# Kernel optimization log

Measured on AMD Instinct MI355X. Metric: run time of the kernel, lower is better.

## Reference

```python
import jax, jax.numpy as jnp
import numpy as np

N, F_IN, HID, NCLS, E = 50000, 128, 256, 40, 600000
BN_EPS = 1e-5


def setup_inputs() -> dict:
    key = jax.random.key(0)
    ks = jax.random.split(key, 12)
    x = jax.random.normal(ks[0], (N, F_IN), dtype=jnp.float32)
    edge_index = jax.random.randint(ks[1], (2, E), 0, N, dtype=jnp.int64)
    # BatchNorm0 (over input features) running stats + affine params
    bn0_gamma = jnp.ones((F_IN,), jnp.float32)
    bn0_beta = jnp.zeros((F_IN,), jnp.float32)
    bn0_mean = jax.random.normal(ks[2], (F_IN,), jnp.float32) * 0.1
    bn0_var = jax.random.uniform(ks[3], (F_IN,), jnp.float32, 0.5, 1.5)
    # GINConv1 linear: F_IN -> HID
    W1 = jax.random.normal(ks[4], (F_IN, HID), jnp.float32) / np.sqrt(F_IN)
    b1 = jnp.zeros((HID,), jnp.float32)
    # BatchNorm1 (over hidden)
    bn1_gamma = jnp.ones((HID,), jnp.float32)
    bn1_beta = jnp.zeros((HID,), jnp.float32)
    bn1_mean = jax.random.normal(ks[5], (HID,), jnp.float32) * 0.1
    bn1_var = jax.random.uniform(ks[6], (HID,), jnp.float32, 0.5, 1.5)
    # GINConv2 linear: HID -> NCLS
    W2 = jax.random.normal(ks[7], (HID, NCLS), jnp.float32) / np.sqrt(HID)
    b2 = jnp.zeros((NCLS,), jnp.float32)
    return {
        "x": x, "edge_index": edge_index,
        "bn0_gamma": bn0_gamma, "bn0_beta": bn0_beta,
        "bn0_mean": bn0_mean, "bn0_var": bn0_var,
        "W1": W1, "b1": b1,
        "bn1_gamma": bn1_gamma, "bn1_beta": bn1_beta,
        "bn1_mean": bn1_mean, "bn1_var": bn1_var,
        "W2": W2, "b2": b2,
    }


def _bn_eval(h, gamma, beta, mean, var):
    return (h - mean) * (gamma / jnp.sqrt(var + BN_EPS)) + beta


def _gin_agg(h, src, dst, n):
    # sum_{j in N(i)} h_j  (scatter-add over edges), plus self term (eps=0)
    return h + jax.ops.segment_sum(h[src], dst, num_segments=n)


def reference(x, edge_index, bn0_gamma, bn0_beta, bn0_mean, bn0_var,
              W1, b1, bn1_gamma, bn1_beta, bn1_mean, bn1_var, W2, b2):
    # Eval mode: dropout / dropout_edge are identity; BN uses running stats.
    src, dst = edge_index[0], edge_index[1]
    n = x.shape[0]
    h = _bn_eval(x, bn0_gamma, bn0_beta, bn0_mean, bn0_var)
    h = _gin_agg(h, src, dst, n) @ W1 + b1          # GINConv1
    h = _bn_eval(h, bn1_gamma, bn1_beta, bn1_mean, bn1_var)
    h = jax.nn.relu(h)
    out = _gin_agg(h, src, dst, n) @ W2 + b2        # GINConv2 -> logits [N, NCLS]
    return out
```

## Files before the change

### kernel.cpp

```cpp
#include <hip/hip_runtime.h>

#define NN 50000
#define FIN 128
#define HID 256
#define NCLS 40
#define NE 600000
#define BN_EPS 1e-5f
#define MAXDEG 64

typedef _Float16 half4_t __attribute__((ext_vector_type(4)));
typedef _Float16 half8_t __attribute__((ext_vector_type(8)));
typedef float float4_t __attribute__((ext_vector_type(4)));


#define OFF_DEG    1600000
#define OFF_GH     1650000
#define OFF_XH     3200000
#define OFF_W1T    6450000
#define OFF_W2T    6466384
#define OFF_P      6472528
#define OFF_Q      6472784
#define OFF_S0V    6473040
#define OFF_S1V    6473168
#define OFF_T0V    6473424

__global__ void scales_k(const float* __restrict__ bn0_g, const float* __restrict__ bn0_b,
                         const float* __restrict__ bn0_m, const float* __restrict__ bn0_v,
                         const float* __restrict__ b1,
                         const float* __restrict__ bn1_g, const float* __restrict__ bn1_b,
                         const float* __restrict__ bn1_m, const float* __restrict__ bn1_v,
                         float* __restrict__ s0v, float* __restrict__ s1v,
                         float* __restrict__ t0v, float* __restrict__ p, float* __restrict__ q) {
    int t = threadIdx.x;
    if (t < FIN) {
        float s = bn0_g[t] * rsqrtf(bn0_v[t] + BN_EPS);
        s0v[t] = s;
        t0v[t] = bn0_b[t] - bn0_m[t] * s;
    }
    float sc = bn1_g[t] * rsqrtf(bn1_v[t] + BN_EPS);
    s1v[t] = sc;
    p[t] = 0.f;
    q[t] = (b1[t] - bn1_m[t]) * sc + bn1_b[t];
}

__global__ void transpose_k(const float* __restrict__ W1, const float* __restrict__ W2,
                            const float* __restrict__ s0v, const float* __restrict__ s1v,
                            const float* __restrict__ t0v,
                            _Float16* __restrict__ W1T, _Float16* __restrict__ W2T,
                            float* __restrict__ p, int* __restrict__ deg) {
    int t = threadIdx.x;
    int b = blockIdx.x;
    if (b >= 9) {
        int i = (b - 9) * 256 + t;
        if (i < NN) deg[i] = 0;
        return;
    }
    if (b < 8) {
        __shared__ _Float16 T[64][65];
        int k0 = (b >> 2) * 64;
        int c0 = (b & 3) * 64;
        int cc = t & 63;
        float psum = 0.f;
        #pragma unroll
        for (int i = 0; i < 16; ++i) {
            int idx = i * 256 + t;
            int kk = idx >> 6;
            float w = W1[(size_t)(k0 + kk) * HID + c0 + cc];
            psum += t0v[k0 + kk] * w;
            T[cc][kk] = (_Float16)(w * s0v[k0 + kk] * s1v[c0 + cc]);
        }
        atomicAdd(&p[c0 + cc], psum * s1v[c0 + cc]);
        __syncthreads();
        #pragma unroll
        for (int i = 0; i < 16; ++i) {
            int idx = i * 256 + t;
            int c2 = idx >> 6, kk2 = idx & 63;
            W1T[(size_t)(c0 + c2) * FIN + k0 + kk2] = T[c2][kk2];
        }
    } else {
        for (int c = 0; c < 48; ++c) {
            float v = (c < NCLS) ? W2[(size_t)t * NCLS + c] : 0.f;
            W2T[(size_t)c * HID + t] = (_Float16)v;
        }
    }
}

__global__ void convert_fill_k(const float4* __restrict__ x4, half4_t* __restrict__ xh4,
                               const int* __restrict__ ei, int* __restrict__ deg,
                               unsigned short* __restrict__ pad) {
    int i = blockIdx.x * 256 + threadIdx.x;
    if (i < NN * 32) {
        float4 v = x4[i];
        half4_t h;
        h[0] = (_Float16)v.x; h[1] = (_Float16)v.y;
        h[2] = (_Float16)v.z; h[3] = (_Float16)v.w;
        xh4[i] = h;
    } else {
        int e = i - NN * 32;
        if (e < NE) {
            int src = ei[e];
            int dst = ei[NE + e];
            int pos = atomicAdd(&deg[dst], 1);
            if (pos < MAXDEG) pad[(size_t)dst * MAXDEG + pos] = (unsigned short)src;
        }
    }
}

__launch_bounds__(256)
__global__ void gather_gemm_k(const half4_t* __restrict__ xh4, const int* __restrict__ deg,
                              const unsigned short* __restrict__ pad,
                              const _Float16* __restrict__ W1T, const _Float16* __restrict__ W2T,
                              const float* __restrict__ p, const float* __restrict__ q,
                              _Float16* __restrict__ gh) {
    __shared__ _Float16 utile[32][136];
    __shared__ _Float16 Htile[32][264];
    __shared__ float scdeg[32];
    int t = threadIdx.x;
    int w = t >> 6, lane = t & 63;
    int lane2 = lane & 31, hw = lane >> 5;
    int node_base = blockIdx.x * 32;

    for (int pr = 0; pr < 4; ++pr) {
        int ln = w * 8 + pr * 2 + hw;
        int n = node_base + ln;
        float ax0 = 0.f, ax1 = 0.f, ax2 = 0.f, ax3 = 0.f;
        int dcnt = 0;
        if (n < NN) {
            dcnt = deg[n];
            if (dcnt > MAXDEG) dcnt = MAXDEG;
            half4_t self = xh4[(size_t)n * 32 + lane2];
            ax0 = (float)self[0]; ax1 = (float)self[1];
            ax2 = (float)self[2]; ax3 = (float)self[3];
        }
        int base = 0;
        while (base < dcnt) {
            int cnt = dcnt - base;
            if (cnt > 32) cnt = 32;
            int vi = (lane2 < cnt) ? (int)pad[(size_t)n * MAXDEG + base + lane2] : 0;
            int j = 0;
            for (; j + 3 < cnt; j += 4) {
                int s0 = __shfl(vi, j, 32), s1 = __shfl(vi, j + 1, 32);
                int s2 = __shfl(vi, j + 2, 32), s3 = __shfl(vi, j + 3, 32);
                half4_t v0 = xh4[(size_t)s0 * 32 + lane2];
                half4_t v1 = xh4[(size_t)s1 * 32 + lane2];
                half4_t v2 = xh4[(size_t)s2 * 32 + lane2];
                half4_t v3 = xh4[(size_t)s3 * 32 + lane2];
                ax0 += (float)v0[0] + (float)v1[0] + (float)v2[0] + (float)v3[0];
                ax1 += (float)v0[1] + (float)v1[1] + (float)v2[1] + (float)v3[1];
                ax2 += (float)v0[2] + (float)v1[2] + (float)v2[2] + (float)v3[2];
                ax3 += (float)v0[3] + (float)v1[3] + (float)v2[3] + (float)v3[3];
            }
            for (; j < cnt; ++j) {
                int s = __shfl(vi, j, 32);
                half4_t v = xh4[(size_t)s * 32 + lane2];
                ax0 += (float)v[0]; ax1 += (float)v[1];
                ax2 += (float)v[2]; ax3 += (float)v[3];
            }
            base += 32;
        }
        half4_t o;
        o[0] = (_Float16)ax0; o[1] = (_Float16)ax1;
        o[2] = (_Float16)ax2; o[3] = (_Float16)ax3;
        *(half4_t*)&utile[ln][lane2 * 4] = o;
        if (lane2 == 0) scdeg[ln] = 1.0f + (float)dcnt;
    }
    __syncthreads();

    int l15 = lane & 15, quad = lane >> 4;
    half8_t a[2][4];
    #pragma unroll
    for (int nb = 0; nb < 2; ++nb)
        #pragma unroll
        for (int ks = 0; ks < 4; ++ks)
            a[nb][ks] = *(const half8_t*)&utile[nb * 16 + l15][ks * 32 + quad * 8];

    #pragma unroll
    for (int ci = 0; ci < 4; ++ci) {
        int ct = w * 4 + ci;
        float4_t acc0 = {0.f, 0.f, 0.f, 0.f};
        float4_t acc1 = {0.f, 0.f, 0.f, 0.f};
        #pragma unroll
        for (int ks = 0; ks < 4; ++ks) {
            half8_t b = *(const half8_t*)(W1T + (size_t)(ct * 16 + l15) * FIN + ks * 32 + quad * 8);
            acc0 = __builtin_amdgcn_mfma_f32_16x16x32_f16(a[0][ks], b, acc0, 0, 0, 0);
            acc1 = __builtin_amdgcn_mfma_f32_16x16x32_f16(a[1][ks], b, acc1, 0, 0, 0);
        }
        int col = ct * 16 + l15;
        float pc = p[col], qc = q[col];
        #pragma unroll
        for (int r = 0; r < 4; ++r) {
            int row = quad * 4 + r;
            float h0 = acc0[r] + scdeg[row] * pc + qc;
            Htile[row][col] = (_Float16)fmaxf(h0, 0.f);
            float h1 = acc1[r] + scdeg[16 + row] * pc + qc;
            Htile[16 + row][col] = (_Float16)fmaxf(h1, 0.f);
        }
    }
    __syncthreads();

    for (int rep = 0; rep < 2; ++rep) {
        int tau = w + rep * 4;
        if (tau >= 6) break;
        int nb = tau / 3, ct2 = tau - nb * 3;
        half8_t a2[8];
        #pragma unroll
        for (int ks = 0; ks < 8; ++ks)
            a2[ks] = *(const half8_t*)&Htile[nb * 16 + l15][ks * 32 + quad * 8];
        float4_t c = {0.f, 0.f, 0.f, 0.f};
        #pragma unroll
        for (int ks = 0; ks < 8; ++ks) {
            half8_t b = *(const half8_t*)(W2T + (size_t)(ct2 * 16 + l15) * HID + ks * 32 + quad * 8);
            c = __builtin_amdgcn_mfma_f32_16x16x32_f16(a2[ks], b, c, 0, 0, 0);
        }
        int col = ct2 * 16 + l15;
        if (col < NCLS) {
            #pragma unroll
            for (int r = 0; r < 4; ++r) {
                int n = node_base + nb * 16 + quad * 4 + r;
                if (n < NN) gh[(size_t)n * NCLS + col] = (_Float16)c[r];
            }
        }
    }
}

__global__ void gather2_k(const _Float16* __restrict__ gh, const int* __restrict__ deg,
                          const unsigned short* __restrict__ pad, const float* __restrict__ b2,
                          float* __restrict__ out) {
    int gid = blockIdx.x * 256 + threadIdx.x;
    int n = gid >> 6, lane = gid & 63;
    if (n >= NN) return;
    int dcnt = deg[n];
    if (dcnt > MAXDEG) dcnt = MAXDEG;
    float acc = 0.f;
    if (lane < NCLS) acc = (float)gh[(size_t)n * NCLS + lane] + b2[lane];
    int vi = (lane < dcnt) ? (int)pad[(size_t)n * MAXDEG + lane] : 0;
    int j = 0;
    for (; j + 3 < dcnt; j += 4) {
        int s0 = __shfl(vi, j), s1 = __shfl(vi, j + 1);
        int s2 = __shfl(vi, j + 2), s3 = __shfl(vi, j + 3);
        if (lane < NCLS) {
            acc += (float)gh[(size_t)s0 * NCLS + lane] + (float)gh[(size_t)s1 * NCLS + lane]
                 + (float)gh[(size_t)s2 * NCLS + lane] + (float)gh[(size_t)s3 * NCLS + lane];
        }
    }
    for (; j < dcnt; ++j) {
        int s = __shfl(vi, j);
        if (lane < NCLS) acc += (float)gh[(size_t)s * NCLS + lane];
    }
    if (lane < NCLS) out[(size_t)n * NCLS + lane] = acc;
}

extern "C" void kernel_launch(void* const* d_in, const int* in_sizes, int n_in,
                              void* d_out, int out_size, void* d_ws, size_t ws_size,
                              hipStream_t stream) {
    const float* x      = (const float*)d_in[0];
    const int*   ei     = (const int*)d_in[1];
    const float* bn0_g  = (const float*)d_in[2];
    const float* bn0_b  = (const float*)d_in[3];
    const float* bn0_m  = (const float*)d_in[4];
    const float* bn0_v  = (const float*)d_in[5];
    const float* W1     = (const float*)d_in[6];
    const float* b1     = (const float*)d_in[7];
    const float* bn1_g  = (const float*)d_in[8];
    const float* bn1_b  = (const float*)d_in[9];
    const float* bn1_m  = (const float*)d_in[10];
    const float* bn1_v  = (const float*)d_in[11];
    const float* W2     = (const float*)d_in[12];
    const float* b2     = (const float*)d_in[13];
    float* out = (float*)d_out;

    float* ws = (float*)d_ws;
    int*   wi = (int*)d_ws;
    unsigned short* pad = (unsigned short*)d_ws;
    int* deg       = wi + OFF_DEG;
    _Float16* gh   = (_Float16*)(ws + OFF_GH);
    _Float16* xh   = (_Float16*)(ws + OFF_XH);
    _Float16* W1T  = (_Float16*)(ws + OFF_W1T);
    _Float16* W2T  = (_Float16*)(ws + OFF_W2T);
    float* p       = ws + OFF_P;
    float* q       = ws + OFF_Q;
    float* s0v     = ws + OFF_S0V;
    float* s1v     = ws + OFF_S1V;
    float* t0v     = ws + OFF_T0V;

    hipLaunchKernelGGL(scales_k, dim3(1), dim3(256), 0, stream,
                       bn0_g, bn0_b, bn0_m, bn0_v, b1,
                       bn1_g, bn1_b, bn1_m, bn1_v, s0v, s1v, t0v, p, q);

    hipLaunchKernelGGL(transpose_k, dim3(9 + 196), dim3(256), 0, stream,
                       W1, W2, s0v, s1v, t0v, W1T, W2T, p, deg);

    hipLaunchKernelGGL(convert_fill_k, dim3((NN * 32 + NE + 255) / 256), dim3(256), 0, stream,
                       (const float4*)x, (half4_t*)xh, ei, deg, pad);

    hipLaunchKernelGGL(gather_gemm_k, dim3((NN + 31) / 32), dim3(256), 0, stream,
                       (const half4_t*)xh, deg, pad, W1T, W2T, p, q, gh);

    hipLaunchKernelGGL(gather2_k, dim3((NN * 64 + 255) / 256), dim3(256), 0, stream,
                       gh, deg, pad, b2, out);
}
```

Before: 210.0 us.

## Fuse scale prep into one kernel and widen gather to half8 with fp16 accumulation

Merges the scales and transpose kernels into one prep kernel that computes the BN scales locally and computes p with a direct per-column loop instead of atomics, removing one launch. The first-layer gather now uses 16 lanes per node with half8 loads and accumulates in packed fp16, with deeper 8-way unrolling and a launch-bounds occupancy hint. The second gather also gets an 8-way unroll. Accumulating neighbour sums in fp16 reduces conversion work but loses precision and risks overflow on high-degree nodes.

```diff
diff --git a/kernel.cpp b/kernel.cpp
--- a/kernel.cpp
+++ b/kernel.cpp
@@ -20,34 +20,15 @@
 #define OFF_W2T    6466384
 #define OFF_P      6472528
 #define OFF_Q      6472784
-#define OFF_S0V    6473040
-#define OFF_S1V    6473168
-#define OFF_T0V    6473424
-
-__global__ void scales_k(const float* __restrict__ bn0_g, const float* __restrict__ bn0_b,
-                         const float* __restrict__ bn0_m, const float* __restrict__ bn0_v,
-                         const float* __restrict__ b1,
-                         const float* __restrict__ bn1_g, const float* __restrict__ bn1_b,
-                         const float* __restrict__ bn1_m, const float* __restrict__ bn1_v,
-                         float* __restrict__ s0v, float* __restrict__ s1v,
-                         float* __restrict__ t0v, float* __restrict__ p, float* __restrict__ q) {
-    int t = threadIdx.x;
-    if (t < FIN) {
-        float s = bn0_g[t] * rsqrtf(bn0_v[t] + BN_EPS);
-        s0v[t] = s;
-        t0v[t] = bn0_b[t] - bn0_m[t] * s;
-    }
-    float sc = bn1_g[t] * rsqrtf(bn1_v[t] + BN_EPS);
-    s1v[t] = sc;
-    p[t] = 0.f;
-    q[t] = (b1[t] - bn1_m[t]) * sc + bn1_b[t];
-}
-
-__global__ void transpose_k(const float* __restrict__ W1, const float* __restrict__ W2,
-                            const float* __restrict__ s0v, const float* __restrict__ s1v,
-                            const float* __restrict__ t0v,
-                            _Float16* __restrict__ W1T, _Float16* __restrict__ W2T,
-                            float* __restrict__ p, int* __restrict__ deg) {
+
+__global__ void prep_k(const float* __restrict__ W1, const float* __restrict__ W2,
+                       const float* __restrict__ bn0_g, const float* __restrict__ bn0_b,
+                       const float* __restrict__ bn0_m, const float* __restrict__ bn0_v,
+                       const float* __restrict__ b1,
+                       const float* __restrict__ bn1_g, const float* __restrict__ bn1_b,
+                       const float* __restrict__ bn1_m, const float* __restrict__ bn1_v,
+                       _Float16* __restrict__ W1T, _Float16* __restrict__ W2T,
+                       float* __restrict__ p, float* __restrict__ q, int* __restrict__ deg) {
     int t = threadIdx.x;
     int b = blockIdx.x;
     if (b >= 9) {
@@ -57,19 +38,23 @@
     }
     if (b < 8) {
         __shared__ _Float16 T[64][65];
+        __shared__ float s0l[64], s1l[64];
         int k0 = (b >> 2) * 64;
         int c0 = (b & 3) * 64;
+        if (t < 64) {
+            s0l[t] = bn0_g[k0 + t] * rsqrtf(bn0_v[k0 + t] + BN_EPS);
+        } else if (t < 128) {
+            int c = t - 64;
+            s1l[c] = bn1_g[c0 + c] * rsqrtf(bn1_v[c0 + c] + BN_EPS);
+        }
+        __syncthreads();
         int cc = t & 63;
-        float psum = 0.f;
         #pragma unroll
         for (int i = 0; i < 16; ++i) {
             int idx = i * 256 + t;
             int kk = idx >> 6;
-            float w = W1[(size_t)(k0 + kk) * HID + c0 + cc];
-            psum += t0v[k0 + kk] * w;
-            T[cc][kk] = (_Float16)(w * s0v[k0 + kk] * s1v[c0 + cc]);
-        }
-        atomicAdd(&p[c0 + cc], psum * s1v[c0 + cc]);
+            T[cc][kk] = (_Float16)(W1[(size_t)(k0 + kk) * HID + c0 + cc] * s0l[kk] * s1l[cc]);
+        }
         __syncthreads();
         #pragma unroll
         for (int i = 0; i < 16; ++i) {
@@ -78,9 +63,20 @@
             W1T[(size_t)(c0 + c2) * FIN + k0 + kk2] = T[c2][kk2];
         }
     } else {
+        __shared__ float t0s[FIN];
+        if (t < FIN) {
+            float s = bn0_g[t] * rsqrtf(bn0_v[t] + BN_EPS);
+            t0s[t] = bn0_b[t] - bn0_m[t] * s;
+        }
+        float sc = bn1_g[t] * rsqrtf(bn1_v[t] + BN_EPS);
+        __syncthreads();
+        float v = 0.f;
+        for (int k = 0; k < FIN; ++k) v += t0s[k] * W1[(size_t)k * HID + t];
+        p[t] = v * sc;
+        q[t] = (b1[t] - bn1_m[t]) * sc + bn1_b[t];
         for (int c = 0; c < 48; ++c) {
-            float v = (c < NCLS) ? W2[(size_t)t * NCLS + c] : 0.f;
-            W2T[(size_t)c * HID + t] = (_Float16)v;
+            float w = (c < NCLS) ? W2[(size_t)t * NCLS + c] : 0.f;
+            W2T[(size_t)c * HID + t] = (_Float16)w;
         }
     }
 }
@@ -106,8 +102,8 @@
     }
 }
 
-__launch_bounds__(256)
-__global__ void gather_gemm_k(const half4_t* __restrict__ xh4, const int* __restrict__ deg,
+__launch_bounds__(256, 6)
+__global__ void gather_gemm_k(const half8_t* __restrict__ xh8, const int* __restrict__ deg,
                               const unsigned short* __restrict__ pad,
                               const _Float16* __restrict__ W1T, const _Float16* __restrict__ W2T,
                               const float* __restrict__ p, const float* __restrict__ q,
@@ -117,52 +113,60 @@
     __shared__ float scdeg[32];
     int t = threadIdx.x;
     int w = t >> 6, lane = t & 63;
-    int lane2 = lane & 31, hw = lane >> 5;
+    int l16 = lane & 15;
+    int qw = lane >> 4;
+    int sbase = lane & 48;
     int node_base = blockIdx.x * 32;
 
-    for (int pr = 0; pr < 4; ++pr) {
-        int ln = w * 8 + pr * 2 + hw;
+    for (int pr = 0; pr < 2; ++pr) {
+        int ln = w * 8 + pr * 4 + qw;
         int n = node_base + ln;
-        float ax0 = 0.f, ax1 = 0.f, ax2 = 0.f, ax3 = 0.f;
+        half8_t acc = {};
         int dcnt = 0;
         if (n < NN) {
-            dcnt = deg[n];
-            if (dcnt > MAXDEG) dcnt = MAXDEG;
-            half4_t self = xh4[(size_t)n * 32 + lane2];
-            ax0 = (float)self[0]; ax1 = (float)self[1];
-            ax2 = (float)self[2]; ax3 = (float)self[3];
+            int d = deg[n];
+            dcnt = d < MAXDEG ? d : MAXDEG;
+            acc = xh8[(size_t)n * 16 + l16];
         }
         int base = 0;
         while (base < dcnt) {
             int cnt = dcnt - base;
-            if (cnt > 32) cnt = 32;
-            int vi = (lane2 < cnt) ? (int)pad[(size_t)n * MAXDEG + base + lane2] : 0;
+            if (cnt > 16) cnt = 16;
+            int vi = (l16 < cnt) ? (int)pad[(size_t)n * MAXDEG + base + l16] : 0;
             int j = 0;
+            for (; j + 7 < cnt; j += 8) {
+                int s0 = __shfl(vi, sbase + j),     s1 = __shfl(vi, sbase + j + 1);
+                int s2 = __shfl(vi, sbase + j + 2), s3 = __shfl(vi, sbase + j + 3);
+                int s4 = __shfl(vi, sbase + j + 4), s5 = __shfl(vi, sbase + j + 5);
+                int s6 = __shfl(vi, sbase + j + 6), s7 = __shfl(vi, sbase + j + 7);
+                half8_t v0 = xh8[(size_t)s0 * 16 + l16];
+                half8_t v1 = xh8[(size_t)s1 * 16 + l16];
+                half8_t v2 = xh8[(size_t)s2 * 16 + l16];
+                half8_t v3 = xh8[(size_t)s3 * 16 + l16];
+                half8_t v4 = xh8[(size_t)s4 * 16 + l16];
+                half8_t v5 = xh8[(size_t)s5 * 16 + l16];
+                half8_t v6 = xh8[(size_t)s6 * 16 + l16];
+                half8_t v7 = xh8[(size_t)s7 * 16 + l16];
+                half8_t t01 = v0 + v1, t23 = v2 + v3, t45 = v4 + v5, t67 = v6 + v7;
+                acc = acc + ((t01 + t23) + (t45 + t67));
+            }
             for (; j + 3 < cnt; j += 4) {
-                int s0 = __shfl(vi, j, 32), s1 = __shfl(vi, j + 1, 32);
-                int s2 = __shfl(vi, j + 2, 32), s3 = __shfl(vi, j + 3, 32);
-                half4_t v0 = xh4[(size_t)s0 * 32 + lane2];
-                half4_t v1 = xh4[(size_t)s1 * 32 + lane2];
-                half4_t v2 = xh4[(size_t)s2 * 32 + lane2];
-                half4_t v3 = xh4[(size_t)s3 * 32 + lane2];
-                ax0 += (float)v0[0] + (float)v1[0] + (float)v2[0] + (float)v3[0];
-                ax1 += (float)v0[1] + (float)v1[1] + (float)v2[1] + (float)v3[1];
-                ax2 += (float)v0[2] + (float)v1[2] + (float)v2[2] + (float)v3[2];
-                ax3 += (float)v0[3] + (float)v1[3] + (float)v2[3] + (float)v3[3];
+                int s0 = __shfl(vi, sbase + j),     s1 = __shfl(vi, sbase + j + 1);
+                int s2 = __shfl(vi, sbase + j + 2), s3 = __shfl(vi, sbase + j + 3);
+                half8_t v0 = xh8[(size_t)s0 * 16 + l16];
+                half8_t v1 = xh8[(size_t)s1 * 16 + l16];
+                half8_t v2 = xh8[(size_t)s2 * 16 + l16];
+                half8_t v3 = xh8[(size_t)s3 * 16 + l16];
+                acc = acc + ((v0 + v1) + (v2 + v3));
             }
             for (; j < cnt; ++j) {
-                int s = __shfl(vi, j, 32);
-                half4_t v = xh4[(size_t)s * 32 + lane2];
-                ax0 += (float)v[0]; ax1 += (float)v[1];
-                ax2 += (float)v[2]; ax3 += (float)v[3];
+                int s = __shfl(vi, sbase + j);
+                acc = acc + xh8[(size_t)s * 16 + l16];
             }
-            base += 32;
-        }
-        half4_t o;
-        o[0] = (_Float16)ax0; o[1] = (_Float16)ax1;
-        o[2] = (_Float16)ax2; o[3] = (_Float16)ax3;
-        *(half4_t*)&utile[ln][lane2 * 4] = o;
-        if (lane2 == 0) scdeg[ln] = 1.0f + (float)dcnt;
+            base += 16;
+        }
+        *(half8_t*)&utile[ln][l16 * 8] = acc;
+        if (l16 == 0) scdeg[ln] = 1.0f + (float)dcnt;
     }
     __syncthreads();
 
@@ -235,12 +239,29 @@
     if (lane < NCLS) acc = (float)gh[(size_t)n * NCLS + lane] + b2[lane];
     int vi = (lane < dcnt) ? (int)pad[(size_t)n * MAXDEG + lane] : 0;
     int j = 0;
+    for (; j + 7 < dcnt; j += 8) {
+        int s0 = __shfl(vi, j),     s1 = __shfl(vi, j + 1);
+        int s2 = __shfl(vi, j + 2), s3 = __shfl(vi, j + 3);
+        int s4 = __shfl(vi, j + 4), s5 = __shfl(vi, j + 5);
+        int s6 = __shfl(vi, j + 6), s7 = __shfl(vi, j + 7);
+        if (lane < NCLS) {
+            float v0 = (float)gh[(size_t)s0 * NCLS + lane];
+            float v1 = (float)gh[(size_t)s1 * NCLS + lane];
+            float v2 = (float)gh[(size_t)s2 * NCLS + lane];
+            float v3 = (float)gh[(size_t)s3 * NCLS + lane];
+            float v4 = (float)gh[(size_t)s4 * NCLS + lane];
+            float v5 = (float)gh[(size_t)s5 * NCLS + lane];
+            float v6 = (float)gh[(size_t)s6 * NCLS + lane];
+            float v7 = (float)gh[(size_t)s7 * NCLS + lane];
+            acc += ((v0 + v1) + (v2 + v3)) + ((v4 + v5) + (v6 + v7));
+        }
+    }
     for (; j + 3 < dcnt; j += 4) {
-        int s0 = __shfl(vi, j), s1 = __shfl(vi, j + 1);
+        int s0 = __shfl(vi, j),     s1 = __shfl(vi, j + 1);
         int s2 = __shfl(vi, j + 2), s3 = __shfl(vi, j + 3);
         if (lane < NCLS) {
-            acc += (float)gh[(size_t)s0 * NCLS + lane] + (float)gh[(size_t)s1 * NCLS + lane]
-                 + (float)gh[(size_t)s2 * NCLS + lane] + (float)gh[(size_t)s3 * NCLS + lane];
+            acc += ((float)gh[(size_t)s0 * NCLS + lane] + (float)gh[(size_t)s1 * NCLS + lane])
+                 + ((float)gh[(size_t)s2 * NCLS + lane] + (float)gh[(size_t)s3 * NCLS + lane]);
         }
     }
     for (; j < dcnt; ++j) {
@@ -279,22 +300,16 @@
     _Float16* W2T  = (_Float16*)(ws + OFF_W2T);
     float* p       = ws + OFF_P;
     float* q       = ws + OFF_Q;
-    float* s0v     = ws + OFF_S0V;
-    float* s1v     = ws + OFF_S1V;
-    float* t0v     = ws + OFF_T0V;
-
-    hipLaunchKernelGGL(scales_k, dim3(1), dim3(256), 0, stream,
-                       bn0_g, bn0_b, bn0_m, bn0_v, b1,
-                       bn1_g, bn1_b, bn1_m, bn1_v, s0v, s1v, t0v, p, q);
-
-    hipLaunchKernelGGL(transpose_k, dim3(9 + 196), dim3(256), 0, stream,
-                       W1, W2, s0v, s1v, t0v, W1T, W2T, p, deg);
+
+    hipLaunchKernelGGL(prep_k, dim3(9 + 196), dim3(256), 0, stream,
+                       W1, W2, bn0_g, bn0_b, bn0_m, bn0_v, b1,
+                       bn1_g, bn1_b, bn1_m, bn1_v, W1T, W2T, p, q, deg);
 
     hipLaunchKernelGGL(convert_fill_k, dim3((NN * 32 + NE + 255) / 256), dim3(256), 0, stream,
                        (const float4*)x, (half4_t*)xh, ei, deg, pad);
 
     hipLaunchKernelGGL(gather_gemm_k, dim3((NN + 31) / 32), dim3(256), 0, stream,
-                       (const half4_t*)xh, deg, pad, W1T, W2T, p, q, gh);
+                       (const half8_t*)xh, deg, pad, W1T, W2T, p, q, gh);
 
     hipLaunchKernelGGL(gather2_k, dim3((NN * 64 + 255) / 256), dim3(256), 0, stream,
                        gh, deg, pad, b2, out);
```

Measured after the change: 213.6 us. No clear change (+1.7%).
